# Kernel optimization log

Measured on AMD Instinct MI355X. Metric: run time of the kernel, lower is better.

The kernel has to match this reference:

```python
import jax, jax.numpy as jnp
import numpy as np

IN_C = 128
OUT_C = 128
KS = (5, 10, 15, 20)  # Chebyshev orders per filter (evenly spaced up to max_chebyshev_order=20)
NUM_FILTERS = len(KS)
LN_EPS = 1e-5


def setup_inputs() -> dict:
    key = jax.random.key(0)
    ks = jax.random.split(key, 10)
    N, E = 50000, 800000
    x = jax.random.normal(ks[0], (N, IN_C), dtype=jnp.float32)
    edge_index = jax.random.randint(ks[1], (2, E), 0, N, dtype=jnp.int64)
    total_K = sum(KS)
    cheb_w = jax.random.normal(ks[2], (total_K, IN_C, OUT_C), dtype=jnp.float32) * (1.0 / np.sqrt(IN_C))
    cheb_b = jax.random.normal(ks[3], (NUM_FILTERS, OUT_C), dtype=jnp.float32) * 0.01
    attn_w = jax.random.normal(ks[4], (NUM_FILTERS * OUT_C, NUM_FILTERS), dtype=jnp.float32) * (1.0 / np.sqrt(NUM_FILTERS * OUT_C))
    attn_b = jnp.zeros((NUM_FILTERS,), dtype=jnp.float32)
    ln_g = jnp.ones((OUT_C,), dtype=jnp.float32)
    ln_b = jnp.zeros((OUT_C,), dtype=jnp.float32)
    return {"x": x, "edge_index": edge_index, "cheb_w": cheb_w, "cheb_b": cheb_b,
            "attn_w": attn_w, "attn_b": attn_b, "ln_g": ln_g, "ln_b": ln_b}


def _scaled_laplacian(edge_index, N, dtype):
    # get_laplacian('sym'): L = I - D^{-1/2} A D^{-1/2}; then (2/lambda_max)*w - 1 with lambda_max=2
    row, col = edge_index[0], edge_index[1]
    w = jnp.ones(row.shape, dtype)
    deg = jax.ops.segment_sum(w, row, num_segments=N)
    dinv = jnp.where(deg > 0, jax.lax.rsqrt(jnp.maximum(deg, 1e-12)), 0.0).astype(dtype)
    lap_w = -dinv[row] * w * dinv[col]          # off-diagonal entries
    loop = jnp.arange(N, dtype=row.dtype)
    src = jnp.concatenate([row, loop])
    dst = jnp.concatenate([col, loop])
    lw = jnp.concatenate([lap_w, jnp.ones((N,), dtype)])  # diagonal = 1
    lw = (2.0 / 2.0) * lw - 1.0                 # faithful: -1 applied to EVERY stored entry
    return src, dst, lw


def _propagate(x, src, dst, w, N):
    # scatter-add of edge-weighted neighbor features (PyG propagate, aggr='add')
    return jax.ops.segment_sum(w[:, None] * x[src], dst, num_segments=N)


def _cheb_conv(x, src, dst, lw, W, b, K, N):
    Tx0 = x
    out = Tx0 @ W[0]
    if K > 1:
        Tx1 = _propagate(x, src, dst, lw, N)
        out = out + Tx1 @ W[1]
        for k in range(2, K):
            Tx2 = 2.0 * _propagate(Tx1, src, dst, lw, N) - Tx0
            out = out + Tx2 @ W[k]
            Tx0, Tx1 = Tx1, Tx2
    return out + b


def reference(x, edge_index, cheb_w, cheb_b, attn_w, attn_b, ln_g, ln_b):
    N = x.shape[0]
    src, dst, lw = _scaled_laplacian(edge_index, N, x.dtype)
    outs = []
    off = 0
    for i, K in enumerate(KS):
        W = cheb_w[off:off + K]
        outs.append(_cheb_conv(x, src, dst, lw, W, cheb_b[i], K, N))
        off += K
    stacked = jnp.stack(outs)                                  # [F, N, C]
    feats = jnp.concatenate(outs, axis=-1)                     # [N, F*C]
    attn = jax.nn.softmax(feats @ attn_w + attn_b, axis=-1)    # [N, F]
    combined = jnp.einsum('nf,fnc->nc', attn, stacked)         # [N, C]
    mu = jnp.mean(combined, axis=-1, keepdims=True)
    var = jnp.mean(jnp.square(combined - mu), axis=-1, keepdims=True)
    return (combined - mu) * jax.lax.rsqrt(var + LN_EPS) * ln_g + ln_b
```

## Files before the change

### kernel.cpp

```cpp
#include <hip/hip_runtime.h>

#define IN_C 128
#define NF 4

typedef __attribute__((ext_vector_type(8))) short short8;
typedef __attribute__((ext_vector_type(4))) float f32x4;

__device__ __forceinline__ unsigned short f2bf(float v) {
    unsigned u = __float_as_uint(v);
    return (unsigned short)((u + 0x7fffu + ((u >> 16) & 1u)) >> 16);
}

__global__ void zero_ints(int* p, int n) {
    int i = blockIdx.x * 256 + threadIdx.x;
    if (i < n) p[i] = 0;
}

__global__ void count_deg(const int* __restrict__ ei, int* __restrict__ degr,
                          int* __restrict__ cnt, int E) {
    int e = blockIdx.x * 256 + threadIdx.x;
    if (e >= E) return;
    atomicAdd(&degr[ei[e]], 1);
    atomicAdd(&cnt[ei[E + e]], 1);
}

__global__ void dinv_k(const int* __restrict__ degr, float* __restrict__ dinv, int N) {
    int i = blockIdx.x * 256 + threadIdx.x;
    if (i >= N) return;
    int d = degr[i];
    dinv[i] = (d > 0) ? rsqrtf((float)d) : 0.0f;
}

__global__ void scanA(const int* __restrict__ in, int* __restrict__ outp,
                      int* __restrict__ partials, int n) {
    __shared__ int tmp[256];
    int t = threadIdx.x;
    int gid = blockIdx.x * 256 + t;
    int v = (gid < n) ? in[gid] : 0;
    tmp[t] = v;
    __syncthreads();
    for (int off = 1; off < 256; off <<= 1) {
        int add = (t >= off) ? tmp[t - off] : 0;
        __syncthreads();
        tmp[t] += add;
        __syncthreads();
    }
    if (gid < n) outp[gid] = tmp[t] - v;
    if (t == 255) partials[blockIdx.x] = tmp[255];
}

__global__ void scanB(int* partials, int n) {
    __shared__ int tmp[256];
    int t = threadIdx.x;
    int v = (t < n) ? partials[t] : 0;
    tmp[t] = v;
    __syncthreads();
    for (int off = 1; off < 256; off <<= 1) {
        int add = (t >= off) ? tmp[t - off] : 0;
        __syncthreads();
        tmp[t] += add;
        __syncthreads();
    }
    if (t < n) partials[t] = tmp[t] - v;
}

__global__ void scanC(int* __restrict__ offs, const int* __restrict__ partials,
                      int n, int total) {
    int gid = blockIdx.x * 256 + threadIdx.x;
    if (gid < n) offs[gid] += partials[blockIdx.x];
    if (gid == 0) offs[n] = total;
}

__global__ void fill_csr(const int* __restrict__ ei, const float* __restrict__ dinv,
                         const int* __restrict__ offs, int* __restrict__ cursor,
                         uint2* __restrict__ csr, int E) {
    int e = blockIdx.x * 256 + threadIdx.x;
    if (e >= E) return;
    int r = ei[e];
    int c = ei[E + e];
    float w = -dinv[r] * dinv[c] - 1.0f;
    int pos = offs[c] + atomicAdd(&cursor[c], 1);
    csr[pos] = make_uint2((unsigned)r, __float_as_uint(w));
}

__global__ void wtr(const float* __restrict__ cheb_w, unsigned short* __restrict__ wht) {
    int gk = blockIdx.x;
    const float* src = cheb_w + (size_t)gk * 16384;
    unsigned short* dst = wht + (size_t)gk * 16384;
    for (int j = 0; j < 64; ++j) {
        int idx = threadIdx.x + j * 256;
        int c = idx >> 7, o = idx & 127;
        dst[o * 128 + c] = f2bf(src[idx]);
    }
}

__global__ void vprep(const float* __restrict__ cheb_w, const float* __restrict__ attn_w,
                      float* __restrict__ V) {
    int k = blockIdx.x;
    int c = threadIdx.x;
    float s[4] = {0.f, 0.f, 0.f, 0.f};
    for (int f = k / 5; f < 4; ++f) {
        const float* wrow = cheb_w + (size_t)((5 * f * (f + 1)) / 2 + k) * 16384 + c * 128;
        const float* arow = attn_w + (size_t)f * 512;
        for (int o = 0; o < 128; ++o) {
            float wv = wrow[o];
            s[0] += wv * arow[o * 4 + 0];
            s[1] += wv * arow[o * 4 + 1];
            s[2] += wv * arow[o * 4 + 2];
            s[3] += wv * arow[o * 4 + 3];
        }
    }
    float* dst = V + k * 512 + c * 4;
    dst[0] = s[0]; dst[1] = s[1]; dst[2] = s[2]; dst[3] = s[3];
}

__global__ void bias_const(const float* __restrict__ cheb_b, const float* __restrict__ attn_w,
                           const float* __restrict__ attn_b, float* __restrict__ constj) {
    int j = threadIdx.x;
    if (j >= 4) return;
    float s = attn_b[j];
    for (int t = 0; t < 512; ++t) s += cheb_b[t] * attn_w[t * 4 + j];
    constj[j] = s;
}

__global__ __launch_bounds__(256) void logit_init(
    const float* __restrict__ x, const float* __restrict__ V,
    const float* __restrict__ constj, float* __restrict__ logits, int N)
{
    int node = blockIdx.x * 4 + (threadIdx.x >> 6);
    int lane = threadIdx.x & 63;
    if (node >= N) return;
    float2 v = ((const float2*)(x + (size_t)node * 128))[lane];
    int cc = lane * 2;
    float4 va = *(const float4*)(V + 4 * cc);
    float4 vb = *(const float4*)(V + 4 * cc + 4);
    float l0 = v.x * va.x + v.y * vb.x;
    float l1 = v.x * va.y + v.y * vb.y;
    float l2 = v.x * va.z + v.y * vb.z;
    float l3 = v.x * va.w + v.y * vb.w;
#pragma unroll
    for (int off = 32; off; off >>= 1) {
        l0 += __shfl_xor(l0, off); l1 += __shfl_xor(l1, off);
        l2 += __shfl_xor(l2, off); l3 += __shfl_xor(l3, off);
    }
    if (lane == 0) {
        float4 cj = *(const float4*)constj;
        *(float4*)(logits + 4 * node) =
            make_float4(l0 + cj.x, l1 + cj.y, l2 + cj.z, l3 + cj.w);
    }
}

__global__ __launch_bounds__(256) void propagate(
    const uint2* __restrict__ csr, const int* __restrict__ offs,
    const float* __restrict__ A, const float* __restrict__ Bsub,
    float* __restrict__ C, float alpha, int N,
    const float* __restrict__ Vk, float* __restrict__ logits)
{
    int node = blockIdx.x * 4 + (threadIdx.x >> 6);
    int lane = threadIdx.x & 63;
    if (node >= N) return;
    int beg = offs[node], end = offs[node + 1];
    float sx = 0.f, sy = 0.f;
    int j = beg;
    for (; j + 3 < end; j += 4) {
        uint2 e0 = csr[j], e1 = csr[j + 1], e2 = csr[j + 2], e3 = csr[j + 3];
        float2 v0 = ((const float2*)(A + (size_t)e0.x * 128))[lane];
        float2 v1 = ((const float2*)(A + (size_t)e1.x * 128))[lane];
        float2 v2 = ((const float2*)(A + (size_t)e2.x * 128))[lane];
        float2 v3 = ((const float2*)(A + (size_t)e3.x * 128))[lane];
        float w0 = __uint_as_float(e0.y), w1 = __uint_as_float(e1.y);
        float w2 = __uint_as_float(e2.y), w3 = __uint_as_float(e3.y);
        sx += w0 * v0.x + w1 * v1.x + w2 * v2.x + w3 * v3.x;
        sy += w0 * v0.y + w1 * v1.y + w2 * v2.y + w3 * v3.y;
    }
    for (; j < end; ++j) {
        uint2 e = csr[j];
        float2 v = ((const float2*)(A + (size_t)e.x * 128))[lane];
        float wv = __uint_as_float(e.y);
        sx += wv * v.x; sy += wv * v.y;
    }
    float ox, oy;
    if (Bsub) {
        float2 b = ((const float2*)(Bsub + (size_t)node * 128))[lane];
        ox = alpha * sx - b.x;
        oy = alpha * sy - b.y;
    } else {
        ox = alpha * sx;
        oy = alpha * sy;
    }
    ((float2*)(C + (size_t)node * 128))[lane] = make_float2(ox, oy);

    int cc = lane * 2;
    float4 va = *(const float4*)(Vk + 4 * cc);
    float4 vb = *(const float4*)(Vk + 4 * cc + 4);
    float l0 = ox * va.x + oy * vb.x;
    float l1 = ox * va.y + oy * vb.y;
    float l2 = ox * va.z + oy * vb.z;
    float l3 = ox * va.w + oy * vb.w;
#pragma unroll
    for (int off = 32; off; off >>= 1) {
        l0 += __shfl_xor(l0, off); l1 += __shfl_xor(l1, off);
        l2 += __shfl_xor(l2, off); l3 += __shfl_xor(l3, off);
    }
    if (lane == 0) {
        float4 cur = *(const float4*)(logits + 4 * node);
        cur.x += l0; cur.y += l1; cur.z += l2; cur.w += l3;
        *(float4*)(logits + 4 * node) = cur;
    }
}

__global__ __launch_bounds__(256) void gemm_mfma(
    const float* __restrict__ x, const float* __restrict__ slots,
    const unsigned short* __restrict__ wht, float* __restrict__ acc_base,
    int N, int g)
{
    __shared__ __align__(16) unsigned short Th[128 * 72];
    __shared__ __align__(16) unsigned short Wh[128 * 72];
    int f = g + blockIdx.y;
    int gk0 = (5 * f * (f + 1)) / 2 + 5 * g;
    float* __restrict__ acc = acc_base + (size_t)f * N * 128;
    int r0 = blockIdx.x * 128;
    int tid = threadIdx.x;
    int wave = tid >> 6, lane = tid & 63;
    int wm = (wave >> 1) * 64, wn = (wave & 1) * 64;
    int quad = lane >> 4, l16 = lane & 15;
    size_t matf = (size_t)N * 128;

    f32x4 dacc[4][4];
#pragma unroll
    for (int a = 0; a < 4; ++a)
#pragma unroll
        for (int b = 0; b < 4; ++b)
#pragma unroll
            for (int e = 0; e < 4; ++e) dacc[a][b][e] = 0.f;

    for (int i = 0; i < 10; ++i) {
        int kl = i >> 1, koff = (i & 1) * 64;
        const float* __restrict__ T = (g == 0 && kl == 0) ? x : slots + (size_t)kl * matf;
        const unsigned short* __restrict__ Wsrc = wht + (size_t)(gk0 + kl) * 16384;
        if (i) __syncthreads();
#pragma unroll
        for (int jj = 0; jj < 8; ++jj) {
            int chunk = tid + jj * 256;
            int r = chunk >> 4, cp = (chunk & 15) * 4;
            int row = r0 + r;
            float4 v = make_float4(0.f, 0.f, 0.f, 0.f);
            if (row < N) v = *(const float4*)(T + (size_t)row * 128 + koff + cp);
            unsigned u0 = (unsigned)f2bf(v.x) | ((unsigned)f2bf(v.y) << 16);
            unsigned u1 = (unsigned)f2bf(v.z) | ((unsigned)f2bf(v.w) << 16);
            *(uint2*)(&Th[r * 72 + cp]) = make_uint2(u0, u1);
        }
#pragma unroll
        for (int jj = 0; jj < 4; ++jj) {
            int chunk = tid + jj * 256;
            int o = chunk >> 3, cp = (chunk & 7) * 8;
            uint4 v = *(const uint4*)(Wsrc + (size_t)o * 128 + koff + cp);
            *(uint4*)(&Wh[o * 72 + cp]) = v;
        }
        __syncthreads();
#pragma unroll
        for (int ks = 0; ks < 64; ks += 32) {
            short8 av[4], bv[4];
#pragma unroll
            for (int mt = 0; mt < 4; ++mt)
                av[mt] = *(const short8*)(&Th[(wm + mt * 16 + l16) * 72 + ks + quad * 8]);
#pragma unroll
            for (int nt = 0; nt < 4; ++nt)
                bv[nt] = *(const short8*)(&Wh[(wn + nt * 16 + l16) * 72 + ks + quad * 8]);
#pragma unroll
            for (int mt = 0; mt < 4; ++mt)
#pragma unroll
                for (int nt = 0; nt < 4; ++nt)
                    dacc[mt][nt] = __builtin_amdgcn_mfma_f32_16x16x32_bf16(
                        av[mt], bv[nt], dacc[mt][nt], 0, 0, 0);
        }
    }
#pragma unroll
    for (int mt = 0; mt < 4; ++mt) {
#pragma unroll
        for (int nt = 0; nt < 4; ++nt) {
            int col = wn + nt * 16 + l16;
#pragma unroll
            for (int e = 0; e < 4; ++e) {
                int row = r0 + wm + mt * 16 + quad * 4 + e;
                if (row < N) {
                    float* p = acc + (size_t)row * 128 + col;
                    float v = dacc[mt][nt][e];
                    if (g > 0) v += *p;
                    *p = v;
                }
            }
        }
    }
}

__global__ __launch_bounds__(256) void attn_ln(
    const float* __restrict__ acc_base, const float* __restrict__ cheb_b,
    const float* __restrict__ logits,
    const float* __restrict__ ln_g, const float* __restrict__ ln_b,
    float* __restrict__ out, int N)
{
    int node = blockIdx.x * 4 + (threadIdx.x >> 6);
    int lane = threadIdx.x & 63;
    if (node >= N) return;
    int c = lane * 2;
    size_t matf = (size_t)N * 128;

    float4 lg = *(const float4*)(logits + 4 * node);
    float m = fmaxf(fmaxf(lg.x, lg.y), fmaxf(lg.z, lg.w));
    float e0 = expf(lg.x - m), e1 = expf(lg.y - m), e2 = expf(lg.z - m), e3 = expf(lg.w - m);
    float inv_s = 1.f / (e0 + e1 + e2 + e3);
    float p[4] = {e0 * inv_s, e1 * inv_s, e2 * inv_s, e3 * inv_s};

    float cx = 0.f, cy = 0.f;
#pragma unroll
    for (int ff = 0; ff < NF; ++ff) {
        float2 v = ((const float2*)(acc_base + (size_t)ff * matf + (size_t)node * 128))[lane];
        cx += p[ff] * (v.x + cheb_b[ff * 128 + c]);
        cy += p[ff] * (v.y + cheb_b[ff * 128 + c + 1]);
    }
    float sum = cx + cy;
#pragma unroll
    for (int off = 32; off; off >>= 1) sum += __shfl_xor(sum, off);
    float mu = sum * (1.f / 128.f);
    float dx = cx - mu, dy = cy - mu;

    float M = fmaxf(fabsf(dx), fabsf(dy));
#pragma unroll
    for (int off = 32; off; off >>= 1) M = fmaxf(M, __shfl_xor(M, off));

    float zx, zy, r;
    if (M > 0.f) {
        float inv = 1.f / M;
        zx = dx * inv; zy = dy * inv;
        float v2 = zx * zx + zy * zy;
#pragma unroll
        for (int off = 32; off; off >>= 1) v2 += __shfl_xor(v2, off);
        float var = v2 * (1.f / 128.f);
        r = rsqrtf(var + 1e-5f * inv * inv);
    } else {
        zx = 0.f; zy = 0.f; r = 0.f;
    }
    out[(size_t)node * 128 + c]     = zx * r * ln_g[c]     + ln_b[c];
    out[(size_t)node * 128 + c + 1] = zy * r * ln_g[c + 1] + ln_b[c + 1];
}

extern "C" void kernel_launch(void* const* d_in, const int* in_sizes, int n_in,
                              void* d_out, int out_size, void* d_ws, size_t ws_size,
                              hipStream_t stream) {
    const float* x       = (const float*)d_in[0];
    const int* ei        = (const int*)d_in[1];
    const float* cheb_w  = (const float*)d_in[2];
    const float* cheb_b  = (const float*)d_in[3];
    const float* attn_w  = (const float*)d_in[4];
    const float* attn_b  = (const float*)d_in[5];
    const float* ln_g    = (const float*)d_in[6];
    const float* ln_b    = (const float*)d_in[7];
    float* out = (float*)d_out;

    int N = in_sizes[0] / 128;
    int E = in_sizes[1] / 2;

    char* w = (char*)d_ws;
    auto alloc = [&](size_t bytes) -> void* {
        void* p = (void*)w;
        w += (bytes + 255) & ~(size_t)255;
        return p;
    };
    size_t mat_bytes = (size_t)N * 128 * sizeof(float);
    float* slots = (float*)alloc(5 * mat_bytes);
    float* acc   = (float*)alloc(4 * mat_bytes);
    uint2* csr   = (uint2*)alloc((size_t)E * sizeof(uint2));
    int* offs    = (int*)alloc((size_t)(N + 1) * sizeof(int));
    int* zero3   = (int*)alloc((size_t)3 * N * sizeof(int));
    int* degr = zero3, *cnt = zero3 + N, *cursor = zero3 + 2 * N;
    float* dinv  = (float*)alloc((size_t)N * sizeof(float));
    int* partials = (int*)alloc(1024 * sizeof(int));
    float* logits = (float*)alloc((size_t)N * 4 * sizeof(float));
    float* V      = (float*)alloc(20 * 512 * sizeof(float));
    float* constj = (float*)alloc(256);
    unsigned short* wht = (unsigned short*)alloc((size_t)50 * 16384 * sizeof(unsigned short));
    if ((size_t)(w - (char*)d_ws) > ws_size) return;

    int eb = (E + 255) / 256;
    int nb = (N + 255) / 256;
    int pb = (N + 3) / 4;
    size_t matf = (size_t)N * 128;

    zero_ints<<<(3 * N + 255) / 256, 256, 0, stream>>>(zero3, 3 * N);
    count_deg<<<eb, 256, 0, stream>>>(ei, degr, cnt, E);
    dinv_k<<<nb, 256, 0, stream>>>(degr, dinv, N);
    scanA<<<nb, 256, 0, stream>>>(cnt, offs, partials, N);
    scanB<<<1, 256, 0, stream>>>(partials, nb);
    scanC<<<nb, 256, 0, stream>>>(offs, partials, N, E);
    fill_csr<<<eb, 256, 0, stream>>>(ei, dinv, offs, cursor, csr, E);

    wtr<<<50, 256, 0, stream>>>(cheb_w, wht);
    vprep<<<20, 128, 0, stream>>>(cheb_w, attn_w, V);
    bias_const<<<1, 64, 0, stream>>>(cheb_b, attn_w, attn_b, constj);
    logit_init<<<pb, 256, 0, stream>>>(x, V, constj, logits, N);

    int rtiles = (N + 127) / 128;
    for (int g = 0; g < 4; ++g) {
        int kbeg = 5 * g + (g == 0 ? 1 : 0);
        int kend = 5 * g + 4;
        for (int k = kbeg; k <= kend; ++k) {
            const float* A = (k == 1) ? x : slots + (size_t)((k - 1) % 5) * matf;
            const float* B = (k == 1) ? nullptr
                            : ((k == 2) ? x : slots + (size_t)((k - 2) % 5) * matf);
            float* C = slots + (size_t)(k % 5) * matf;
            propagate<<<pb, 256, 0, stream>>>(csr, offs, A, B, C,
                                              (k == 1) ? 1.f : 2.f, N,
                                              V + k * 512, logits);
        }
        dim3 grid(rtiles, 4 - g);
        gemm_mfma<<<grid, 256, 0, stream>>>(x, slots, wht, acc, N, g);
    }
    attn_ln<<<pb, 256, 0, stream>>>(acc, cheb_b, logits, ln_g, ln_b, out, N);
}
```

Baseline: 1.920 ms.

## Emit bf16 copies of Chebyshev terms in propagate and feed GEMM from them

Propagate now writes a bf16 copy of each Chebyshev term alongside the fp32 one, and the MFMA GEMM loads these bf16 tiles directly instead of reading fp32 and converting. This halves the GEMM's input traffic and removes per-tile conversion work. The fp32 ring shrinks to three slots, which is all the recurrence needs. Propagate also changes layout: each half-wave gathers a different edge using float4 loads, with 8 edges in flight per iteration, and the halves are combined with a cross-lane shuffle. Only half the lanes store, and the extra bf16 write adds some traffic to propagate.

```diff
diff --git a/kernel.cpp b/kernel.cpp
--- a/kernel.cpp
+++ b/kernel.cpp
@@ -125,13 +125,17 @@
 
 __global__ __launch_bounds__(256) void logit_init(
     const float* __restrict__ x, const float* __restrict__ V,
-    const float* __restrict__ constj, float* __restrict__ logits, int N)
+    const float* __restrict__ constj, float* __restrict__ logits,
+    unsigned short* __restrict__ xb, int N)
 {
     int node = blockIdx.x * 4 + (threadIdx.x >> 6);
     int lane = threadIdx.x & 63;
     if (node >= N) return;
     float2 v = ((const float2*)(x + (size_t)node * 128))[lane];
     int cc = lane * 2;
+    unsigned u = (unsigned)f2bf(v.x) | ((unsigned)f2bf(v.y) << 16);
+    *(unsigned*)(xb + (size_t)node * 128 + cc) = u;
+
     float4 va = *(const float4*)(V + 4 * cc);
     float4 vb = *(const float4*)(V + 4 * cc + 4);
     float l0 = v.x * va.x + v.y * vb.x;
@@ -153,52 +157,65 @@
 __global__ __launch_bounds__(256) void propagate(
     const uint2* __restrict__ csr, const int* __restrict__ offs,
     const float* __restrict__ A, const float* __restrict__ Bsub,
-    float* __restrict__ C, float alpha, int N,
+    float* __restrict__ C, unsigned short* __restrict__ Cb,
+    float alpha, int N,
     const float* __restrict__ Vk, float* __restrict__ logits)
 {
     int node = blockIdx.x * 4 + (threadIdx.x >> 6);
     int lane = threadIdx.x & 63;
     if (node >= N) return;
+    int half = lane >> 5;
+    int cl = (lane & 31) * 4;
     int beg = offs[node], end = offs[node + 1];
-    float sx = 0.f, sy = 0.f;
-    int j = beg;
-    for (; j + 3 < end; j += 4) {
-        uint2 e0 = csr[j], e1 = csr[j + 1], e2 = csr[j + 2], e3 = csr[j + 3];
-        float2 v0 = ((const float2*)(A + (size_t)e0.x * 128))[lane];
-        float2 v1 = ((const float2*)(A + (size_t)e1.x * 128))[lane];
-        float2 v2 = ((const float2*)(A + (size_t)e2.x * 128))[lane];
-        float2 v3 = ((const float2*)(A + (size_t)e3.x * 128))[lane];
-        float w0 = __uint_as_float(e0.y), w1 = __uint_as_float(e1.y);
-        float w2 = __uint_as_float(e2.y), w3 = __uint_as_float(e3.y);
-        sx += w0 * v0.x + w1 * v1.x + w2 * v2.x + w3 * v3.x;
-        sy += w0 * v0.y + w1 * v1.y + w2 * v2.y + w3 * v3.y;
-    }
-    for (; j < end; ++j) {
-        uint2 e = csr[j];
-        float2 v = ((const float2*)(A + (size_t)e.x * 128))[lane];
-        float wv = __uint_as_float(e.y);
-        sx += wv * v.x; sy += wv * v.y;
-    }
-    float ox, oy;
+
+    float4 s = make_float4(0.f, 0.f, 0.f, 0.f);
+    for (int j = beg; j < end; j += 8) {
+        uint2 e[4];
+        float4 v[4];
+#pragma unroll
+        for (int u = 0; u < 4; ++u) {
+            int je = j + 2 * u + half;
+            e[u] = (je < end) ? csr[je] : make_uint2(0u, 0u);
+        }
+#pragma unroll
+        for (int u = 0; u < 4; ++u)
+            v[u] = *(const float4*)(A + (size_t)e[u].x * 128 + cl);
+#pragma unroll
+        for (int u = 0; u < 4; ++u) {
+            float wv = __uint_as_float(e[u].y);
+            s.x += wv * v[u].x; s.y += wv * v[u].y;
+            s.z += wv * v[u].z; s.w += wv * v[u].w;
+        }
+    }
+    s.x += __shfl_xor(s.x, 32); s.y += __shfl_xor(s.y, 32);
+    s.z += __shfl_xor(s.z, 32); s.w += __shfl_xor(s.w, 32);
+
+    float4 o;
     if (Bsub) {
-        float2 b = ((const float2*)(Bsub + (size_t)node * 128))[lane];
-        ox = alpha * sx - b.x;
-        oy = alpha * sy - b.y;
+        float4 b = *(const float4*)(Bsub + (size_t)node * 128 + cl);
+        o.x = alpha * s.x - b.x; o.y = alpha * s.y - b.y;
+        o.z = alpha * s.z - b.z; o.w = alpha * s.w - b.w;
     } else {
-        ox = alpha * sx;
-        oy = alpha * sy;
-    }
-    ((float2*)(C + (size_t)node * 128))[lane] = make_float2(ox, oy);
-
-    int cc = lane * 2;
-    float4 va = *(const float4*)(Vk + 4 * cc);
-    float4 vb = *(const float4*)(Vk + 4 * cc + 4);
-    float l0 = ox * va.x + oy * vb.x;
-    float l1 = ox * va.y + oy * vb.y;
-    float l2 = ox * va.z + oy * vb.z;
-    float l3 = ox * va.w + oy * vb.w;
-#pragma unroll
-    for (int off = 32; off; off >>= 1) {
+        o.x = alpha * s.x; o.y = alpha * s.y;
+        o.z = alpha * s.z; o.w = alpha * s.w;
+    }
+    if (half == 0) {
+        *(float4*)(C + (size_t)node * 128 + cl) = o;
+        unsigned u0 = (unsigned)f2bf(o.x) | ((unsigned)f2bf(o.y) << 16);
+        unsigned u1 = (unsigned)f2bf(o.z) | ((unsigned)f2bf(o.w) << 16);
+        *(uint2*)(Cb + (size_t)node * 128 + cl) = make_uint2(u0, u1);
+    }
+
+    float4 w0 = *(const float4*)(Vk + 4 * cl);
+    float4 w1 = *(const float4*)(Vk + 4 * (cl + 1));
+    float4 w2 = *(const float4*)(Vk + 4 * (cl + 2));
+    float4 w3 = *(const float4*)(Vk + 4 * (cl + 3));
+    float l0 = o.x * w0.x + o.y * w1.x + o.z * w2.x + o.w * w3.x;
+    float l1 = o.x * w0.y + o.y * w1.y + o.z * w2.y + o.w * w3.y;
+    float l2 = o.x * w0.z + o.y * w1.z + o.z * w2.z + o.w * w3.z;
+    float l3 = o.x * w0.w + o.y * w1.w + o.z * w2.w + o.w * w3.w;
+#pragma unroll
+    for (int off = 16; off; off >>= 1) {
         l0 += __shfl_xor(l0, off); l1 += __shfl_xor(l1, off);
         l2 += __shfl_xor(l2, off); l3 += __shfl_xor(l3, off);
     }
@@ -210,7 +227,7 @@
 }
 
 __global__ __launch_bounds__(256) void gemm_mfma(
-    const float* __restrict__ x, const float* __restrict__ slots,
+    const unsigned short* __restrict__ xb, const unsigned short* __restrict__ Tb,
     const unsigned short* __restrict__ wht, float* __restrict__ acc_base,
     int N, int g)
 {
@@ -236,19 +253,18 @@
 
     for (int i = 0; i < 10; ++i) {
         int kl = i >> 1, koff = (i & 1) * 64;
-        const float* __restrict__ T = (g == 0 && kl == 0) ? x : slots + (size_t)kl * matf;
+        const unsigned short* __restrict__ Tsrc =
+            (g == 0 && kl == 0) ? xb : Tb + (size_t)kl * matf;
         const unsigned short* __restrict__ Wsrc = wht + (size_t)(gk0 + kl) * 16384;
         if (i) __syncthreads();
 #pragma unroll
-        for (int jj = 0; jj < 8; ++jj) {
+        for (int jj = 0; jj < 4; ++jj) {
             int chunk = tid + jj * 256;
-            int r = chunk >> 4, cp = (chunk & 15) * 4;
+            int r = chunk >> 3, cp = (chunk & 7) * 8;
             int row = r0 + r;
-            float4 v = make_float4(0.f, 0.f, 0.f, 0.f);
-            if (row < N) v = *(const float4*)(T + (size_t)row * 128 + koff + cp);
-            unsigned u0 = (unsigned)f2bf(v.x) | ((unsigned)f2bf(v.y) << 16);
-            unsigned u1 = (unsigned)f2bf(v.z) | ((unsigned)f2bf(v.w) << 16);
-            *(uint2*)(&Th[r * 72 + cp]) = make_uint2(u0, u1);
+            uint4 v = make_uint4(0u, 0u, 0u, 0u);
+            if (row < N) v = *(const uint4*)(Tsrc + (size_t)row * 128 + koff + cp);
+            *(uint4*)(&Th[r * 72 + cp]) = v;
         }
 #pragma unroll
         for (int jj = 0; jj < 4; ++jj) {
@@ -367,9 +383,12 @@
         w += (bytes + 255) & ~(size_t)255;
         return p;
     };
-    size_t mat_bytes = (size_t)N * 128 * sizeof(float);
-    float* slots = (float*)alloc(5 * mat_bytes);
-    float* acc   = (float*)alloc(4 * mat_bytes);
+    size_t matf = (size_t)N * 128;
+    size_t mat_bytes = matf * sizeof(float);
+    float* slots3 = (float*)alloc(3 * mat_bytes);
+    float* acc    = (float*)alloc(4 * mat_bytes);
+    unsigned short* Tb = (unsigned short*)alloc(5 * matf * sizeof(unsigned short));
+    unsigned short* xb = (unsigned short*)alloc(matf * sizeof(unsigned short));
     uint2* csr   = (uint2*)alloc((size_t)E * sizeof(uint2));
     int* offs    = (int*)alloc((size_t)(N + 1) * sizeof(int));
     int* zero3   = (int*)alloc((size_t)3 * N * sizeof(int));
@@ -385,7 +404,6 @@
     int eb = (E + 255) / 256;
     int nb = (N + 255) / 256;
     int pb = (N + 3) / 4;
-    size_t matf = (size_t)N * 128;
 
     zero_ints<<<(3 * N + 255) / 256, 256, 0, stream>>>(zero3, 3 * N);
     count_deg<<<eb, 256, 0, stream>>>(ei, degr, cnt, E);
@@ -398,23 +416,24 @@
     wtr<<<50, 256, 0, stream>>>(cheb_w, wht);
     vprep<<<20, 128, 0, stream>>>(cheb_w, attn_w, V);
     bias_const<<<1, 64, 0, stream>>>(cheb_b, attn_w, attn_b, constj);
-    logit_init<<<pb, 256, 0, stream>>>(x, V, constj, logits, N);
+    logit_init<<<pb, 256, 0, stream>>>(x, V, constj, logits, xb, N);
 
     int rtiles = (N + 127) / 128;
     for (int g = 0; g < 4; ++g) {
         int kbeg = 5 * g + (g == 0 ? 1 : 0);
         int kend = 5 * g + 4;
         for (int k = kbeg; k <= kend; ++k) {
-            const float* A = (k == 1) ? x : slots + (size_t)((k - 1) % 5) * matf;
+            const float* A = (k == 1) ? x : slots3 + (size_t)((k - 1) % 3) * matf;
             const float* B = (k == 1) ? nullptr
-                            : ((k == 2) ? x : slots + (size_t)((k - 2) % 5) * matf);
-            float* C = slots + (size_t)(k % 5) * matf;
-            propagate<<<pb, 256, 0, stream>>>(csr, offs, A, B, C,
+                            : ((k == 2) ? x : slots3 + (size_t)((k - 2) % 3) * matf);
+            float* C = slots3 + (size_t)(k % 3) * matf;
+            unsigned short* Cb = Tb + (size_t)(k % 5) * matf;
+            propagate<<<pb, 256, 0, stream>>>(csr, offs, A, B, C, Cb,
                                               (k == 1) ? 1.f : 2.f, N,
                                               V + k * 512, logits);
         }
         dim3 grid(rtiles, 4 - g);
-        gemm_mfma<<<grid, 256, 0, stream>>>(x, slots, wht, acc, N, g);
+        gemm_mfma<<<grid, 256, 0, stream>>>(xb, Tb, wht, acc, N, g);
     }
     attn_ln<<<pb, 256, 0, stream>>>(acc, cheb_b, logits, ln_g, ln_b, out, N);
 }
```

Result: faster. 1.856 ms (-3.3%).
